# Kernel tuning notes

Measured on AMD Instinct MI355X. Metric: run time of the kernel, lower is better.

## Reference

```python
import jax, jax.numpy as jnp
import numpy as np

D_MODEL = 1024

def setup_inputs() -> dict:
    key = jax.random.key(0)
    ks = jax.random.split(key, 7)
    B, T, D = 4, 4096, D_MODEL
    s = 1.0 / np.sqrt(D)
    return {
        "x": jax.random.normal(ks[0], (B, T, D), dtype=jnp.float32),
        "Wq": jax.random.normal(ks[1], (D, D), dtype=jnp.float32) * s,
        "bq": jax.random.normal(ks[2], (D,), dtype=jnp.float32) * 0.01,
        "Wk": jax.random.normal(ks[3], (D, D), dtype=jnp.float32) * s,
        "bk": jax.random.normal(ks[4], (D,), dtype=jnp.float32) * 0.01,
        "Wv": jax.random.normal(ks[5], (D, D), dtype=jnp.float32) * s,
        "bv": jax.random.normal(ks[6], (D,), dtype=jnp.float32) * 0.01,
    }

def reference(x, Wq, bq, Wk, bk, Wv, bv):
    # x: [B, T, D]; Linear weights stored [out, in] like torch -> x @ W.T + b
    D = x.shape[-1]
    T = x.shape[1]
    scale = jnp.sqrt(jnp.asarray(D, dtype=x.dtype))
    Q = jnp.einsum('btd,ed->bte', x, Wq) + bq
    K = jnp.einsum('btd,ed->bte', x, Wk) + bk
    V = jnp.einsum('btd,ed->bte', x, Wv) + bv
    scores = jnp.einsum('bqd,bkd->bqk', Q, K) / scale  # [B, T, T]
    causal = jnp.tril(jnp.ones((T, T), dtype=bool))    # True = keep (q >= k)
    neg_inf = jnp.asarray(-jnp.inf, dtype=scores.dtype)
    scores = jnp.where(causal, scores, neg_inf)
    probs = jax.nn.softmax(scores, axis=-1)
    return jnp.einsum('bqk,bkd->bqd', probs, V)
```

## Files before the change

kernel.cpp:

```cpp
#include <hip/hip_runtime.h>
#include <hip/hip_bf16.h>
#include <math.h>


typedef __bf16 bf16;
typedef __bf16 bf16x8 __attribute__((ext_vector_type(8)));
typedef float  f32x4  __attribute__((ext_vector_type(4)));

#define LOG2E 1.4426950408889634f

static constexpr size_t OFF_XB   = 0;
static constexpr size_t OFF_WQB  = 33554432;
static constexpr size_t OFF_WKB  = 35651584;
static constexpr size_t OFF_WVB  = 37748736;
static constexpr size_t OFF_Q    = 39845888;
static constexpr size_t OFF_K    = 73400320;
static constexpr size_t OFF_VT   = 106954752;
static constexpr size_t OFF_S    = 140509184;
static constexpr size_t OFF_PSUM = 209715200;
static constexpr size_t OFF_LINV = 211812352;

typedef __attribute__((address_space(1))) void gvoid_t;
typedef __attribute__((address_space(3))) void lvoid_t;

__device__ __forceinline__ void gload16(const void* g, void* l) {
  __builtin_amdgcn_global_load_lds((gvoid_t*)g, (lvoid_t*)l, 16, 0, 0);
}

struct Ctx { int tid, lane, quad, col16, wr, wc, wcol; };
__device__ __forceinline__ Ctx mk_ctx() {
  Ctx c; c.tid = (int)threadIdx.x; c.lane = c.tid & 63;
  int w = c.tid >> 6;
  c.quad = c.lane >> 4; c.col16 = c.lane & 15;
  c.wr = (w >> 1) * 64; c.wc = (w & 1) * 64; c.wcol = w & 1;
  return c;
}

__device__ __forceinline__ void stage_tile(const bf16* g, long ld, bf16* s, int tid) {
  int lane = tid & 63, w = tid >> 6;
  const bf16* gp = g + (long)(lane >> 2) * ld + (long)(lane & 3) * 8;
  long step = 16 * ld;
  gload16(gp + (long)(2 * w) * step,     s + (2 * w) * 512);
  gload16(gp + (long)(2 * w + 1) * step, s + (2 * w + 1) * 512);
}

__device__ __forceinline__ void mfma_step(const bf16* sA, const bf16* sB,
                                          const Ctx& c, f32x4 acc[4][4]) {
  bf16x8 a[4], b[4];
#pragma unroll
  for (int i = 0; i < 4; ++i) {
    a[i] = *(const bf16x8*)(sA + ((c.wr + i * 16 + c.col16) * 32 + c.quad * 8));
    b[i] = *(const bf16x8*)(sB + ((c.wc + i * 16 + c.col16) * 32 + c.quad * 8));
  }
#pragma unroll
  for (int i = 0; i < 4; ++i)
#pragma unroll
    for (int j = 0; j < 4; ++j)
      acc[i][j] = __builtin_amdgcn_mfma_f32_16x16x32_bf16(a[i], b[j], acc[i][j], 0, 0, 0);
}

__device__ __forceinline__ void zero_acc(f32x4 acc[4][4]) {
  f32x4 z = {0.f, 0.f, 0.f, 0.f};
#pragma unroll
  for (int i = 0; i < 4; ++i)
#pragma unroll
    for (int j = 0; j < 4; ++j) acc[i][j] = z;
}

__device__ __forceinline__ int tridec(int i) {
  int qt = (int)((sqrtf(8.0f * (float)i + 1.0f) - 1.0f) * 0.5f);
  while ((qt + 1) * (qt + 2) / 2 <= i) ++qt;
  while (qt * (qt + 1) / 2 > i) --qt;
  return qt;
}


__global__ __launch_bounds__(256) void cvt_all(const float* __restrict__ x,
                                               const float* __restrict__ Wq,
                                               const float* __restrict__ Wk,
                                               const float* __restrict__ Wv,
                                               bf16* __restrict__ xb,
                                               bf16* __restrict__ wqb,
                                               bf16* __restrict__ wkb,
                                               bf16* __restrict__ wvb) {
  int b = (int)blockIdx.x;
  const float* in; bf16* out; long base;
  if (b < 8192)      { in = x;  out = xb;  base = (long)b * 2048; }
  else if (b < 8704) { in = Wq; out = wqb; base = (long)(b - 8192) * 2048; }
  else if (b < 9216) { in = Wk; out = wkb; base = (long)(b - 8704) * 2048; }
  else               { in = Wv; out = wvb; base = (long)(b - 9216) * 2048; }
  long i = base + (long)threadIdx.x * 8;
  float4 f0 = *(const float4*)(in + i);
  float4 f1 = *(const float4*)(in + i + 4);
  bf16x8 h;
  h[0] = (bf16)f0.x; h[1] = (bf16)f0.y; h[2] = (bf16)f0.z; h[3] = (bf16)f0.w;
  h[4] = (bf16)f1.x; h[5] = (bf16)f1.y; h[6] = (bf16)f1.z; h[7] = (bf16)f1.w;
  *(bf16x8*)(out + i) = h;
}

__global__ __launch_bounds__(256) void qkv_gemm(const bf16* __restrict__ X,
                                                const bf16* __restrict__ Wq,
                                                const bf16* __restrict__ Wk,
                                                const bf16* __restrict__ Wv,
                                                const float* __restrict__ bq,
                                                const float* __restrict__ bk,
                                                const float* __restrict__ bv,
                                                bf16* __restrict__ Q,
                                                bf16* __restrict__ K,
                                                bf16* __restrict__ Vt) {
  __shared__ __align__(16) bf16 sA[2][128 * 32], sB[2][128 * 32];
  Ctx c = mk_ctx();
  int b = (int)blockIdx.x;
  const bf16 *Ag, *Bg;
  bool is_vt = (b >= 2048);
  long r0, c0;
  if (!is_vt) {
    int isK = (b >> 10) & 1, rem = b & 1023;
    c0 = (long)(rem & 7) * 128;
    r0 = (long)(rem >> 3) * 128;
    Ag = X + r0 * 1024;
    Bg = (isK ? Wk : Wq) + c0 * 1024;
  } else {
    int vb = b - 2048;
    int z = vb & 3, e = (vb >> 2) & 7, t = vb >> 5;
    r0 = (long)e * 128;
    c0 = (long)t * 128;
    Ag = Wv + r0 * 1024;
    Bg = X + (long)z * 4194304 + c0 * 1024;
  }
  f32x4 acc[4][4]; zero_acc(acc);
  for (int k = 0; k < 1024; k += 64) {
    stage_tile(Ag + k,      1024, sA[0], c.tid);
    stage_tile(Ag + k + 32, 1024, sA[1], c.tid);
    stage_tile(Bg + k,      1024, sB[0], c.tid);
    stage_tile(Bg + k + 32, 1024, sB[1], c.tid);
    __syncthreads();
    mfma_step(sA[0], sB[0], c, acc);
    mfma_step(sA[1], sB[1], c, acc);
    __syncthreads();
  }
  if (!is_vt) {
    int isK = (b >> 10) & 1;
    const float* bias = isK ? bk : bq;
    bf16* out = isK ? K : Q;
#pragma unroll
    for (int j = 0; j < 4; ++j) {
      int col = c.wc + j * 16 + c.col16;
      float bb = bias[c0 + col];
#pragma unroll
      for (int i = 0; i < 4; ++i) {
        int rowb = c.wr + i * 16 + c.quad * 4;
#pragma unroll
        for (int r = 0; r < 4; ++r)
          out[(r0 + rowb + r) * 1024 + c0 + col] = (bf16)(acc[i][j][r] + bb);
      }
    }
  } else {
    int vb = b - 2048;
    int z = vb & 3;
    bf16* out = Vt + (long)z * 4194304;
#pragma unroll
    for (int i = 0; i < 4; ++i) {
      int rowb = c.wr + i * 16 + c.quad * 4;
      float bb[4];
#pragma unroll
      for (int r = 0; r < 4; ++r) bb[r] = bv[r0 + rowb + r];
#pragma unroll
      for (int j = 0; j < 4; ++j) {
        int col = c.wc + j * 16 + c.col16;
#pragma unroll
        for (int r = 0; r < 4; ++r)
          out[(r0 + rowb + r) * 4096 + c0 + col] = (bf16)(acc[i][j][r] + bb[r]);
      }
    }
  }
}

__global__ __launch_bounds__(256) void s_gemm(const bf16* __restrict__ Q,
                                              const bf16* __restrict__ K,
                                              bf16* __restrict__ S,
                                              float* __restrict__ psum) {
  __shared__ __align__(16) bf16 sA[2][128 * 32], sB[2][128 * 32];
  __shared__ float sred[2][128];
  Ctx c = mk_ctx();
  int ti = blockIdx.x, z = blockIdx.z;
  int qt = tridec(ti);
  int kt = ti - qt * (qt + 1) / 2;
  long q0 = (long)qt * 128, k0 = (long)kt * 128;
  const bf16* Ab = Q + (long)z * 4194304 + q0 * 1024;
  const bf16* Bb = K + (long)z * 4194304 + k0 * 1024;
  f32x4 acc[4][4]; zero_acc(acc);
  for (int k = 0; k < 1024; k += 64) {
    stage_tile(Ab + k,      1024, sA[0], c.tid);
    stage_tile(Ab + k + 32, 1024, sA[1], c.tid);
    stage_tile(Bb + k,      1024, sB[0], c.tid);
    stage_tile(Bb + k + 32, 1024, sB[1], c.tid);
    __syncthreads();
    mfma_step(sA[0], sB[0], c, acc);
    mfma_step(sA[1], sB[1], c, acc);
    __syncthreads();
  }
  bf16* st = S + ((long)z * 528 + ti) * 16384;
  const bool diag = (qt == kt);
  float rs[4][4];
#pragma unroll
  for (int i = 0; i < 4; ++i) {
#pragma unroll
    for (int r = 0; r < 4; ++r) {
      int row_l = c.wr + i * 16 + c.quad * 4 + r;
      float s = 0.f;
#pragma unroll
      for (int j = 0; j < 4; ++j) {
        int col_l = c.wc + j * 16 + c.col16;
        float p = exp2f(acc[i][j][r] * (0.03125f * LOG2E));
        if (diag && col_l > row_l) p = 0.0f;
        bf16 h = (bf16)p;
        st[row_l * 128 + col_l] = h;
        s += (float)h;
      }
      rs[i][r] = s;
    }
  }
#pragma unroll
  for (int i = 0; i < 4; ++i)
#pragma unroll
    for (int r = 0; r < 4; ++r)
#pragma unroll
      for (int m = 1; m <= 8; m <<= 1)
        rs[i][r] += __shfl_xor(rs[i][r], m);
  if (c.col16 == 0) {
#pragma unroll
    for (int i = 0; i < 4; ++i)
#pragma unroll
      for (int r = 0; r < 4; ++r)
        sred[c.wcol][c.wr + i * 16 + c.quad * 4 + r] = rs[i][r];
  }
  __syncthreads();
  if (c.tid < 128)
    psum[((long)z * 4096 + q0 + c.tid) * 32 + kt] = sred[0][c.tid] + sred[1][c.tid];
}

__global__ __launch_bounds__(256) void inv_sums(const float* __restrict__ psum,
                                                float* __restrict__ linv) {
  long i = (long)blockIdx.x * 256 + threadIdx.x;
  int q = (int)(i & 4095);
  int nt = (q >> 7) + 1;
  const float* ps = psum + i * 32;
  float l = 0.f;
  for (int t = 0; t < nt; ++t) l += ps[t];
  linv[i] = 1.0f / l;
}

__global__ __launch_bounds__(256) void o_gemm(const bf16* __restrict__ S,
                                              const bf16* __restrict__ Vt,
                                              const float* __restrict__ linv,
                                              float* __restrict__ out) {
  __shared__ __align__(16) bf16 sA[2][128 * 32], sB[2][128 * 32];
  Ctx c = mk_ctx();
  int b = (int)blockIdx.x;
  int z = b & 3, et = (b >> 2) & 7, q0i = (b >> 5) & 7, gen = b >> 8;
  int qt = (gen == 0) ? q0i : (gen == 1) ? 15 - q0i
         : (gen == 2) ? 16 + q0i : 31 - q0i;
  long q0 = (long)qt * 128, e0 = (long)et * 128;
  const bf16* Bb = Vt + (long)z * 4194304 + e0 * 4096;
  long tribase = ((long)z * 528 + (long)qt * (qt + 1) / 2) * 16384;
  f32x4 acc[4][4]; zero_acc(acc);
  int kend = (qt + 1) * 128;
  for (int k = 0; k < kend; k += 64) {
    const bf16* Ab = S + tribase + (long)(k >> 7) * 16384 + (k & 127);
    stage_tile(Ab,      128, sA[0], c.tid);
    stage_tile(Ab + 32, 128, sA[1], c.tid);
    stage_tile(Bb + k,      4096, sB[0], c.tid);
    stage_tile(Bb + k + 32, 4096, sB[1], c.tid);
    __syncthreads();
    mfma_step(sA[0], sB[0], c, acc);
    mfma_step(sA[1], sB[1], c, acc);
    __syncthreads();
  }
  long zq = (long)z * 4096 + q0;
#pragma unroll
  for (int i = 0; i < 4; ++i) {
    int rowb = c.wr + i * 16 + c.quad * 4;
    float li[4];
#pragma unroll
    for (int r = 0; r < 4; ++r) li[r] = linv[zq + rowb + r];
#pragma unroll
    for (int j = 0; j < 4; ++j) {
      int col = c.wc + j * 16 + c.col16;
#pragma unroll
      for (int r = 0; r < 4; ++r)
        out[(zq + rowb + r) * 1024 + e0 + col] = acc[i][j][r] * li[r];
    }
  }
}

extern "C" void kernel_launch(void* const* d_in, const int* in_sizes, int n_in,
                              void* d_out, int out_size, void* d_ws, size_t ws_size,
                              hipStream_t stream) {
  (void)in_sizes; (void)n_in; (void)out_size; (void)ws_size;
  const float* x  = (const float*)d_in[0];
  const float* Wq = (const float*)d_in[1];
  const float* bq = (const float*)d_in[2];
  const float* Wk = (const float*)d_in[3];
  const float* bk = (const float*)d_in[4];
  const float* Wv = (const float*)d_in[5];
  const float* bv = (const float*)d_in[6];

  char* ws = (char*)d_ws;
  bf16*  xb   = (bf16*)(ws + OFF_XB);
  bf16*  wqb  = (bf16*)(ws + OFF_WQB);
  bf16*  wkb  = (bf16*)(ws + OFF_WKB);
  bf16*  wvb  = (bf16*)(ws + OFF_WVB);
  bf16*  Qb   = (bf16*)(ws + OFF_Q);
  bf16*  Kb   = (bf16*)(ws + OFF_K);
  bf16*  Vtb  = (bf16*)(ws + OFF_VT);
  bf16*  Sb   = (bf16*)(ws + OFF_S);
  float* psum = (float*)(ws + OFF_PSUM);
  float* linv = (float*)(ws + OFF_LINV);

  cvt_all<<<9728, 256, 0, stream>>>(x, Wq, Wk, Wv, xb, wqb, wkb, wvb);
  qkv_gemm<<<3072, 256, 0, stream>>>(xb, wqb, wkb, wvb, bq, bk, bv, Qb, Kb, Vtb);
  s_gemm<<<dim3(528, 1, 4), 256, 0, stream>>>(Qb, Kb, Sb, psum);
  inv_sums<<<64, 256, 0, stream>>>(psum, linv);
  o_gemm<<<1024, 256, 0, stream>>>(Sb, Vtb, linv, (float*)d_out);
}
```

Baseline: 509.0 us.

## Rewrite QKV projection GEMM with 256x256 tiles and software-pipelined LDS staging

After: 486.6 us. 1.05x faster.

```diff
diff --git a/kernel.cpp b/kernel.cpp
--- a/kernel.cpp
+++ b/kernel.cpp
@@ -27,6 +27,14 @@
   __builtin_amdgcn_global_load_lds((gvoid_t*)g, (lvoid_t*)l, 16, 0, 0);
 }
 
+#define PRIO1() __builtin_amdgcn_s_setprio(1)
+#define PRIO0() __builtin_amdgcn_s_setprio(0)
+#define BAR()   __builtin_amdgcn_s_barrier()
+#define LGKM0() asm volatile("s_waitcnt lgkmcnt(0)" ::: "memory")
+#define LGKM8() asm volatile("s_waitcnt lgkmcnt(8)" ::: "memory")
+#define VM0()   asm volatile("s_waitcnt vmcnt(0)" ::: "memory")
+#define VM4()   asm volatile("s_waitcnt vmcnt(4)" ::: "memory")
+
 struct Ctx { int tid, lane, quad, col16, wr, wc, wcol; };
 __device__ __forceinline__ Ctx mk_ctx() {
   Ctx c; c.tid = (int)threadIdx.x; c.lane = c.tid & 63;
@@ -72,6 +80,139 @@
   while ((qt + 1) * (qt + 2) / 2 <= i) ++qt;
   while (qt * (qt + 1) / 2 > i) --qt;
   return qt;
+}
+
+struct CC { int soff, raOff, rbOff, lofs; };
+__device__ __forceinline__ CC mk_cc(int tid) {
+  CC c;
+  int lane = tid & 63, w = tid >> 6;
+  int quad = lane >> 4, col16 = lane & 15;
+  int wrow = (w >> 2) << 7, wcol = (w & 3) << 6;
+  c.soff = ((tid >> 3) << 10) + (((tid & 7) ^ (((tid >> 5) & 1) << 1)) << 3);
+  int cS = (quad << 3) ^ (((col16 >> 2) & 1) << 4);
+  c.raOff = ((wrow + col16) << 6) + cS;
+  c.rbOff = ((wcol + col16) << 6) + cS;
+  c.lofs = w << 9;
+  return c;
+}
+
+__device__ __forceinline__ void stg(const bf16* g, int kofs, bf16* l, const CC& c) {
+  const bf16* g0 = g + kofs + c.soff;
+  gload16(g0,         l + c.lofs);
+  gload16(g0 + 65536, l + c.lofs + 4096);
+}
+
+__device__ __forceinline__ void read_a(const bf16* buf, const CC& c, int h, bf16x8 a[8]) {
+#pragma unroll
+  for (int f = 0; f < 4; ++f)
+#pragma unroll
+    for (int kk = 0; kk < 2; ++kk)
+      a[f * 2 + kk] = *(const bf16x8*)(buf + c.raOff + h * 4096 + f * 1024 + kk * 32);
+}
+
+__device__ __forceinline__ void read_b(const bf16* buf, const CC& c, int cc, bf16x8 bb[4]) {
+#pragma unroll
+  for (int g = 0; g < 2; ++g)
+#pragma unroll
+    for (int kk = 0; kk < 2; ++kk)
+      bb[g * 2 + kk] = *(const bf16x8*)(buf + c.rbOff + cc * 2048 + g * 1024 + kk * 32);
+}
+
+__device__ __forceinline__ void mfma16(const bf16x8 a[8], const bf16x8 bb[4],
+                                       int h, int cc, f32x4 acc[8][4]) {
+#pragma unroll
+  for (int f = 0; f < 4; ++f)
+#pragma unroll
+    for (int g = 0; g < 2; ++g)
+#pragma unroll
+      for (int kk = 0; kk < 2; ++kk)
+        acc[h * 4 + f][cc * 2 + g] = __builtin_amdgcn_mfma_f32_16x16x32_bf16(
+            a[f * 2 + kk], bb[g * 2 + kk], acc[h * 4 + f][cc * 2 + g], 0, 0, 0);
+}
+
+__device__ __forceinline__ void zero8x4(f32x4 acc[8][4]) {
+  f32x4 z = {0.f, 0.f, 0.f, 0.f};
+#pragma unroll
+  for (int i = 0; i < 8; ++i)
+#pragma unroll
+    for (int j = 0; j < 4; ++j) acc[i][j] = z;
+}
+
+template <int NT>
+__device__ __forceinline__ void gemm256_core(const bf16* __restrict__ Ag,
+                                             const bf16* __restrict__ Bg,
+                                             bf16* sA0, bf16* sA1,
+                                             bf16* sB0, bf16* sB1,
+                                             const CC& c, f32x4 acc[8][4]) {
+  stg(Ag, 0,           sA0, c); stg(Ag, 131072,      sA0 + 8192, c);
+  stg(Bg, 0,           sB0, c); stg(Bg, 131072,      sB0 + 8192, c);
+  stg(Bg, 64,          sB1, c); stg(Bg, 64 + 131072, sB1 + 8192, c);
+  VM4(); BAR();
+
+  bf16x8 a[8], b0[4], b1[4];
+#pragma unroll 1
+  for (int i = 0; i < NT / 2 - 1; ++i) {
+    const int k1 = (2 * i + 1) << 6, k2 = k1 + 64, k3 = k1 + 128;
+    read_a(sA0, c, 0, a); read_b(sB0, c, 0, b0);
+    stg(Ag, k1, sA1, c);
+    LGKM8(); BAR(); LGKM0();
+    PRIO1(); mfma16(a, b0, 0, 0, acc); PRIO0(); BAR();
+    read_b(sB0, c, 1, b1);
+    stg(Ag, k1 + 131072, sA1 + 8192, c);
+    BAR(); LGKM0();
+    PRIO1(); mfma16(a, b1, 0, 1, acc); PRIO0(); BAR();
+    read_a(sA0, c, 1, a);
+    stg(Bg, k2, sB0, c);
+    BAR(); LGKM0();
+    PRIO1(); mfma16(a, b1, 1, 1, acc); PRIO0(); BAR();
+    stg(Bg, k2 + 131072, sB0 + 8192, c);
+    BAR();
+    PRIO1(); mfma16(a, b0, 1, 0, acc); PRIO0();
+    VM4(); BAR();
+    read_a(sA1, c, 0, a); read_b(sB1, c, 0, b0);
+    stg(Ag, k2, sA0, c);
+    LGKM8(); BAR(); LGKM0();
+    PRIO1(); mfma16(a, b0, 0, 0, acc); PRIO0(); BAR();
+    read_b(sB1, c, 1, b1);
+    stg(Ag, k2 + 131072, sA0 + 8192, c);
+    BAR(); LGKM0();
+    PRIO1(); mfma16(a, b1, 0, 1, acc); PRIO0(); BAR();
+    read_a(sA1, c, 1, a);
+    stg(Bg, k3, sB1, c);
+    BAR(); LGKM0();
+    PRIO1(); mfma16(a, b1, 1, 1, acc); PRIO0(); BAR();
+    stg(Bg, k3 + 131072, sB1 + 8192, c);
+    BAR();
+    PRIO1(); mfma16(a, b0, 1, 0, acc); PRIO0();
+    VM4(); BAR();
+  }
+  {
+    const int k1 = (NT - 1) << 6;
+    read_a(sA0, c, 0, a); read_b(sB0, c, 0, b0);
+    stg(Ag, k1, sA1, c);
+    LGKM8(); BAR(); LGKM0();
+    PRIO1(); mfma16(a, b0, 0, 0, acc); PRIO0(); BAR();
+    read_b(sB0, c, 1, b1);
+    stg(Ag, k1 + 131072, sA1 + 8192, c);
+    BAR(); LGKM0();
+    PRIO1(); mfma16(a, b1, 0, 1, acc); PRIO0(); BAR();
+    read_a(sA0, c, 1, a);
+    BAR(); LGKM0();
+    PRIO1(); mfma16(a, b1, 1, 1, acc); PRIO0(); BAR();
+    BAR();
+    PRIO1(); mfma16(a, b0, 1, 0, acc); PRIO0();
+    VM0(); BAR();
+    read_a(sA1, c, 0, a); read_b(sB1, c, 0, b0);
+    LGKM8(); BAR(); LGKM0();
+    PRIO1(); mfma16(a, b0, 0, 0, acc); PRIO0(); BAR();
+    read_b(sB1, c, 1, b1);
+    BAR(); LGKM0();
+    PRIO1(); mfma16(a, b1, 0, 1, acc); PRIO0(); BAR();
+    read_a(sA1, c, 1, a);
+    BAR(); LGKM0();
+    PRIO1(); mfma16(a, b1, 1, 1, acc); PRIO0();
+    mfma16(a, b0, 1, 0, acc);
+  }
 }
 
 
@@ -98,79 +239,73 @@
   *(bf16x8*)(out + i) = h;
 }
 
-__global__ __launch_bounds__(256) void qkv_gemm(const bf16* __restrict__ X,
-                                                const bf16* __restrict__ Wq,
-                                                const bf16* __restrict__ Wk,
-                                                const bf16* __restrict__ Wv,
-                                                const float* __restrict__ bq,
-                                                const float* __restrict__ bk,
-                                                const float* __restrict__ bv,
-                                                bf16* __restrict__ Q,
-                                                bf16* __restrict__ K,
-                                                bf16* __restrict__ Vt) {
-  __shared__ __align__(16) bf16 sA[2][128 * 32], sB[2][128 * 32];
-  Ctx c = mk_ctx();
-  int b = (int)blockIdx.x;
+__global__ __launch_bounds__(512, 2) void qkv_gemm(const bf16* __restrict__ X,
+                                                   const bf16* __restrict__ Wq,
+                                                   const bf16* __restrict__ Wk,
+                                                   const bf16* __restrict__ Wv,
+                                                   const float* __restrict__ bq,
+                                                   const float* __restrict__ bk,
+                                                   const float* __restrict__ bv,
+                                                   bf16* __restrict__ Q,
+                                                   bf16* __restrict__ K,
+                                                   bf16* __restrict__ Vt) {
+  __shared__ __align__(16) bf16 lds[4][16384];
+  const int tid = (int)threadIdx.x;
+  const CC c = mk_cc(tid);
+  int b0i = (int)blockIdx.x;
+  int b = (b0i & 7) * 96 + (b0i >> 3);
   const bf16 *Ag, *Bg;
-  bool is_vt = (b >= 2048);
-  long r0, c0;
+  const bool is_vt = (b >= 512);
   if (!is_vt) {
-    int isK = (b >> 10) & 1, rem = b & 1023;
-    c0 = (long)(rem & 7) * 128;
-    r0 = (long)(rem >> 3) * 128;
-    Ag = X + r0 * 1024;
-    Bg = (isK ? Wk : Wq) + c0 * 1024;
+    int isK = b >> 8, rem = b & 255;
+    Ag = X + (long)(rem >> 2) * 262144;
+    Bg = (isK ? Wk : Wq) + (long)(rem & 3) * 262144;
   } else {
-    int vb = b - 2048;
-    int z = vb & 3, e = (vb >> 2) & 7, t = vb >> 5;
-    r0 = (long)e * 128;
-    c0 = (long)t * 128;
-    Ag = Wv + r0 * 1024;
-    Bg = X + (long)z * 4194304 + c0 * 1024;
-  }
-  f32x4 acc[4][4]; zero_acc(acc);
-  for (int k = 0; k < 1024; k += 64) {
-    stage_tile(Ag + k,      1024, sA[0], c.tid);
-    stage_tile(Ag + k + 32, 1024, sA[1], c.tid);
-    stage_tile(Bg + k,      1024, sB[0], c.tid);
-    stage_tile(Bg + k + 32, 1024, sB[1], c.tid);
-    __syncthreads();
-    mfma_step(sA[0], sB[0], c, acc);
-    mfma_step(sA[1], sB[1], c, acc);
-    __syncthreads();
-  }
+    int rem = b - 512;
+    Ag = Wv + (long)((rem >> 4) & 3) * 262144;
+    Bg = X + (long)(rem >> 6) * 4194304 + (long)(rem & 15) * 262144;
+  }
+  f32x4 acc[8][4];
+  zero8x4(acc);
+  gemm256_core<16>(Ag, Bg, lds[0], lds[1], lds[2], lds[3], c, acc);
+
+  const int lane = tid & 63, w = tid >> 6;
+  const int quad = lane >> 4, col16 = lane & 15;
+  const int wrow = (w >> 2) << 7, wcol = (w & 3) << 6;
   if (!is_vt) {
-    int isK = (b >> 10) & 1;
+    int isK = b >> 8, rem = b & 255;
+    long r0 = (long)(rem >> 2) * 256, c0 = (long)(rem & 3) * 256;
     const float* bias = isK ? bk : bq;
     bf16* out = isK ? K : Q;
 #pragma unroll
-    for (int j = 0; j < 4; ++j) {
-      int col = c.wc + j * 16 + c.col16;
-      float bb = bias[c0 + col];
-#pragma unroll
-      for (int i = 0; i < 4; ++i) {
-        int rowb = c.wr + i * 16 + c.quad * 4;
+    for (int n = 0; n < 4; ++n) {
+      int col = (int)c0 + wcol + (n >> 1) * 32 + (n & 1) * 16 + col16;
+      float bb = bias[col];
+#pragma unroll
+      for (int m = 0; m < 8; ++m) {
+        long rowb = r0 + wrow + (m >> 2) * 64 + (m & 3) * 16 + quad * 4;
 #pragma unroll
         for (int r = 0; r < 4; ++r)
-          out[(r0 + rowb + r) * 1024 + c0 + col] = (bf16)(acc[i][j][r] + bb);
+          out[(rowb + r) * 1024 + col] = (bf16)(acc[m][n][r] + bb);
       }
     }
   } else {
-    int vb = b - 2048;
-    int z = vb & 3;
+    int rem = b - 512;
+    int z = rem >> 6;
+    long r0 = (long)((rem >> 4) & 3) * 256, c0 = (long)(rem & 15) * 256;
     bf16* out = Vt + (long)z * 4194304;
 #pragma unroll
-    for (int i = 0; i < 4; ++i) {
-      int rowb = c.wr + i * 16 + c.quad * 4;
+    for (int m = 0; m < 8; ++m) {
+      long rowb = r0 + wrow + (m >> 2) * 64 + (m & 3) * 16 + quad * 4;
       float bb[4];
 #pragma unroll
-      for (int r = 0; r < 4; ++r) bb[r] = bv[r0 + rowb + r];
-#pragma unroll
-      for (int j = 0; j < 4; ++j) {
-        int col = c.wc + j * 16 + c.col16;
+      for (int r = 0; r < 4; ++r) bb[r] = bv[rowb + r];
+#pragma unroll
+      for (int n = 0; n < 4; ++n) {
+        int col = (int)c0 + wcol + (n >> 1) * 32 + (n & 1) * 16 + col16;
 #pragma unroll
         for (int r = 0; r < 4; ++r)
-          out[(r0 + rowb + r) * 4096 + c0 + col] = (bf16)(acc[i][j][r] + bb[r]);
+          out[(rowb + r) * 4096 + col] = (bf16)(acc[m][n][r] + bb[r]);
       }
     }
   }
@@ -319,7 +454,7 @@
   float* linv = (float*)(ws + OFF_LINV);
 
   cvt_all<<<9728, 256, 0, stream>>>(x, Wq, Wk, Wv, xb, wqb, wkb, wvb);
-  qkv_gemm<<<3072, 256, 0, stream>>>(xb, wqb, wkb, wvb, bq, bk, bv, Qb, Kb, Vtb);
+  qkv_gemm<<<768, 512, 0, stream>>>(xb, wqb, wkb, wvb, bq, bk, bv, Qb, Kb, Vtb);
   s_gemm<<<dim3(528, 1, 4), 256, 0, stream>>>(Qb, Kb, Sb, psum);
   inv_sums<<<64, 256, 0, stream>>>(psum, linv);
   o_gemm<<<1024, 256, 0, stream>>>(Sb, Vtb, linv, (float*)d_out);
```
